# Performance work log

Measured on AMD Instinct MI355X. Metric: run time of the kernel, lower is better.

## Reference

```python
import jax, jax.numpy as jnp
import numpy as np


def _skew(w):
    # w: (..., 3) -> (..., 3, 3)
    wx, wy, wz = w[..., 0], w[..., 1], w[..., 2]
    z = jnp.zeros_like(wx)
    return jnp.stack([
        jnp.stack([z, -wz, wy], axis=-1),
        jnp.stack([wz, z, -wx], axis=-1),
        jnp.stack([-wy, wx, z], axis=-1),
    ], axis=-2)


def exp_se3(xi):
    # xi: (..., 6) se(3) coordinates [w, v] -> (..., 4, 4) SE(3) matrix exponential
    w = xi[..., :3]
    v = xi[..., 3:]
    th2 = jnp.sum(w * w, axis=-1)
    small = th2 < 1e-12
    th2_safe = jnp.where(small, 1.0, th2)
    th = jnp.sqrt(th2_safe)
    # Rodrigues coefficients with small-angle Taylor fallbacks
    A = jnp.where(small, 1.0 - th2 / 6.0, jnp.sin(th) / th)
    B = jnp.where(small, 0.5 - th2 / 24.0, (1.0 - jnp.cos(th)) / th2_safe)
    C = jnp.where(small, 1.0 / 6.0 - th2 / 120.0, (th - jnp.sin(th)) / (th2_safe * th))
    W = _skew(w)
    W2 = W @ W
    I3 = jnp.eye(3, dtype=xi.dtype)
    R = I3 + A[..., None, None] * W + B[..., None, None] * W2
    V = I3 + B[..., None, None] * W + C[..., None, None] * W2
    p = jnp.einsum('...ij,...j->...i', V, v)
    top = jnp.concatenate([R, p[..., None]], axis=-1)            # (..., 3, 4)
    bottom_row = jnp.array([0.0, 0.0, 0.0, 1.0], dtype=xi.dtype)
    bot = jnp.broadcast_to(bottom_row, top.shape[:-2] + (1, 4))  # (..., 1, 4)
    return jnp.concatenate([top, bot], axis=-2)


def setup_inputs() -> dict:
    key = jax.random.key(0)
    k1, k2, k3 = jax.random.split(key, 3)
    nBatch, nJoint = 262144, 24
    x = jax.random.normal(k1, (nBatch, nJoint), dtype=jnp.float32)
    # eta ~ U(-1, 1) per torch init (stdv = 1)
    eta = jax.random.uniform(k2, (nJoint, 6), dtype=jnp.float32, minval=-1.0, maxval=1.0)
    # M_se3 ~ U(-2, 2)
    M_se3 = jax.random.uniform(k3, (1, 6), dtype=jnp.float32, minval=-2.0, maxval=2.0)
    return {"x": x, "eta": eta, "M_se3": M_se3}


def reference(x, eta, M_se3):
    # x: (B, nJoint) joint angles; eta: (nJoint, 6) joint twists (useAdjoint=False);
    # M_se3: (1, 6) home pose in se(3).
    nBatch = x.shape[0]
    joint_twist = eta  # getJointTwist() with useAdjoint=False

    def step(T, inp):
        twist, ang = inp                                  # (6,), (B,)
        E = exp_se3(ang[:, None] * twist[None, :])        # (B, 4, 4)
        return T @ E, None

    T0 = jnp.broadcast_to(jnp.eye(4, dtype=x.dtype), (nBatch, 4, 4))
    T, _ = jax.lax.scan(step, T0, (joint_twist, x.T))
    return T @ exp_se3(M_se3)  # (B,4,4) @ (1,4,4) broadcasts over batch
```

## Files before the change

kernel.cpp:

```cpp
#include <hip/hip_runtime.h>

#define NJ   24
#define BLK  256
#define JREC 5
#define QMF4 (NJ * JREC)
#define NCPY (NJ * JREC + 2)
#define INV4PI 0.07957747154594767f

__global__ __launch_bounds__(BLK, 8)
void poe_main(const float* __restrict__ x,
              const float* __restrict__ eta,
              const float* __restrict__ M,
              float* __restrict__ out,
              int nBatch)
{
    __shared__ float4 sC[NCPY];
    float* sF = (float*)sC;

    const int t = threadIdx.x;
    if (t < NJ) {
        const float w0 = eta[t*6+0], w1 = eta[t*6+1], w2 = eta[t*6+2];
        const float v0 = eta[t*6+3], v1 = eta[t*6+4], v2 = eta[t*6+5];
        const float k  = w0*w0 + w1*w1 + w2*w2;
        const bool  sm = (k < 1e-12f);
        const float invsqk = sm ? 0.0f : rsqrtf(k);
        const float sqk    = k * invsqk;
        const float invk   = invsqk * invsqk;
        const float invk15 = invk * invsqk;
        const float c10 = w1*v2 - w2*v1;
        const float c11 = w2*v0 - w0*v2;
        const float c12 = w0*v1 - w1*v0;
        const float c20 = w1*c12 - w2*c11;
        const float c21 = w2*c10 - w0*c12;
        const float c22 = w0*c11 - w1*c10;
        float* r = sF + t * JREC * 4;
        r[0]  = w0*invsqk;  r[1]  = w1*invsqk;  r[2]  = w2*invsqk;  r[3]  = sqk;
        r[4]  = v0;         r[5]  = v1;         r[6]  = v2;         r[7]  = sqk * INV4PI;
        r[8]  = c10*invk;   r[9]  = c11*invk;   r[10] = c12*invk;   r[11] = 0.0f;
        r[12] = c20*invk15; r[13] = c21*invk15; r[14] = c22*invk15; r[15] = 0.0f;
    } else if (t == NJ) {
        const float w0 = M[0], w1 = M[1], w2 = M[2];
        const float v0 = M[3], v1 = M[4], v2 = M[5];
        const float t2 = w0*w0 + w1*w1 + w2*w2;
        const bool  sm = (t2 < 1e-12f);
        const float t2s  = sm ? 1.0f : t2;
        const float invt = rsqrtf(t2s);
        const float th   = t2s * invt;
        float s, c;
        __sincosf(th, &s, &c);
        const float invt2 = invt * invt;
        const float B = sm ? 0.5f        : (1.0f - c) * invt2;
        const float C = sm ? (1.0f/6.0f) : (th - s) * invt2 * invt;
        float sh, chh;
        __sincosf(0.5f * th, &sh, &chh);
        const float axs = sm ? 0.5f : sh * invt;
        float* r = sF + QMF4 * 4;
        r[0] = sm ? 1.0f : chh;
        r[1] = axs * w0;
        r[2] = axs * w1;
        r[3] = axs * w2;
        const float c10 = w1*v2 - w2*v1, c11 = w2*v0 - w0*v2, c12 = w0*v1 - w1*v0;
        const float c20 = w1*c12 - w2*c11, c21 = w2*c10 - w0*c12, c22 = w0*c11 - w1*c10;
        r[4] = v0 + B*c10 + C*c20;
        r[5] = v1 + B*c11 + C*c21;
        r[6] = v2 + B*c12 + C*c22;
        r[7] = 0.0f;
    }

    const int gid = blockIdx.x * BLK + t;
    const int row = gid >> 2;
    const int q   = gid & 3;
    const bool active = row < nBatch;

    float2 xa = make_float2(0.f,0.f), xb = xa, xc = xa;
    if (active) {
        const float2* xp = (const float2*)(x + (size_t)row * NJ + q * 6);
        xa = xp[0]; xb = xp[1]; xc = xp[2];
    }

    __syncthreads();

    float Qw=1.f, Qx=0.f, Qy=0.f, Qz=0.f;
    float p0=0.f, p1=0.f, p2=0.f;

    const int cbase = q * 6 * JREC;

#define JSTEP(JJ, A_) do {                                                    \
    const float4 A4 = sC[cbase + (JJ)*JREC + 0];                              \
    const float4 B4 = sC[cbase + (JJ)*JREC + 1];                              \
    const float4 C4 = sC[cbase + (JJ)*JREC + 2];                              \
    const float4 D4 = sC[cbase + (JJ)*JREC + 3];                              \
    const float a    = (A_);                                                  \
    const float hrev = a * B4.w;                                              \
    const float sh   = __builtin_amdgcn_sinf(hrev);                           \
    const float ch   = __builtin_amdgcn_cosf(hrev);                           \
    const float s    = 2.0f * sh * ch;                        \
    const float cB   = 2.0f * sh * sh;                        \
    const float phi  = a * A4.w;                                              \
    const float g    = phi - s;                                               \
    const float qj0 = fmaf(a, B4.x, fmaf(cB, C4.x, g * D4.x));                \
    const float qj1 = fmaf(a, B4.y, fmaf(cB, C4.y, g * D4.y));                \
    const float qj2 = fmaf(a, B4.z, fmaf(cB, C4.z, g * D4.z));                \
    const float u10 = Qy*qj2 - Qz*qj1;                                        \
    const float u11 = Qz*qj0 - Qx*qj2;                                        \
    const float u12 = Qx*qj1 - Qy*qj0;                                        \
    const float u20 = Qy*u12 - Qz*u11;                                        \
    const float u21 = Qz*u10 - Qx*u12;                                        \
    const float u22 = Qx*u11 - Qy*u10;                                        \
    const float tw  = 2.0f * Qw;                                              \
    p0 = fmaf(tw, u10, fmaf(2.0f, u20, p0 + qj0));                            \
    p1 = fmaf(tw, u11, fmaf(2.0f, u21, p1 + qj1));                            \
    p2 = fmaf(tw, u12, fmaf(2.0f, u22, p2 + qj2));                            \
    const float ex = sh * A4.x, ey = sh * A4.y, ez = sh * A4.z;               \
    const float nQw = Qw*ch - Qx*ex - Qy*ey - Qz*ez;                          \
    const float nQx = Qw*ex + Qx*ch + Qy*ez - Qz*ey;                          \
    const float nQy = Qw*ey - Qx*ez + Qy*ch + Qz*ex;                          \
    const float nQz = Qw*ez + Qx*ey - Qy*ex + Qz*ch;                          \
    Qw=nQw; Qx=nQx; Qy=nQy; Qz=nQz;                                           \
} while (0)

    JSTEP(0, xa.x); JSTEP(1, xa.y); JSTEP(2, xb.x);
    JSTEP(3, xb.y); JSTEP(4, xc.x); JSTEP(5, xc.y);
#undef JSTEP

#define COMBINE(BIT) do {                                                     \
    const float oQw = __shfl_xor(Qw, BIT), oQx = __shfl_xor(Qx, BIT);         \
    const float oQy = __shfl_xor(Qy, BIT), oQz = __shfl_xor(Qz, BIT);         \
    const float op0 = __shfl_xor(p0, BIT), op1 = __shfl_xor(p1, BIT);         \
    const float op2 = __shfl_xor(p2, BIT);                                    \
    const bool up = (q & (BIT)) != 0;          \
    const float Aw = up ? oQw : Qw, Ax = up ? oQx : Qx;                       \
    const float Ay = up ? oQy : Qy, Az = up ? oQz : Qz;                       \
    const float Ap0 = up ? op0 : p0, Ap1 = up ? op1 : p1, Ap2 = up ? op2 : p2;\
    const float Bw = up ? Qw : oQw, Bx = up ? Qx : oQx;                       \
    const float By = up ? Qy : oQy, Bz = up ? Qz : oQz;                       \
    const float Bp0 = up ? p0 : op0, Bp1 = up ? p1 : op1, Bp2 = up ? p2 : op2;\
    const float u10 = Ay*Bp2 - Az*Bp1;                                        \
    const float u11 = Az*Bp0 - Ax*Bp2;                                        \
    const float u12 = Ax*Bp1 - Ay*Bp0;                                        \
    const float u20 = Ay*u12 - Az*u11;                                        \
    const float u21 = Az*u10 - Ax*u12;                                        \
    const float u22 = Ax*u11 - Ay*u10;                                        \
    const float tw  = 2.0f * Aw;                                              \
    p0 = fmaf(tw, u10, fmaf(2.0f, u20, Ap0 + Bp0));                           \
    p1 = fmaf(tw, u11, fmaf(2.0f, u21, Ap1 + Bp1));                           \
    p2 = fmaf(tw, u12, fmaf(2.0f, u22, Ap2 + Bp2));                           \
    Qw = Aw*Bw - Ax*Bx - Ay*By - Az*Bz;                                       \
    Qx = Aw*Bx + Ax*Bw + Ay*Bz - Az*By;                                       \
    Qy = Aw*By - Ax*Bz + Ay*Bw + Az*Bx;                                       \
    Qz = Aw*Bz + Ax*By - Ay*Bx + Az*Bw;                                       \
} while (0)

    COMBINE(1);
    COMBINE(2);
#undef COMBINE

    {
        const float4 Qm = sC[QMF4];
        const float4 Pm = sC[QMF4 + 1];
        const float u10 = Qy*Pm.z - Qz*Pm.y;
        const float u11 = Qz*Pm.x - Qx*Pm.z;
        const float u12 = Qx*Pm.y - Qy*Pm.x;
        const float u20 = Qy*u12 - Qz*u11;
        const float u21 = Qz*u10 - Qx*u12;
        const float u22 = Qx*u11 - Qy*u10;
        const float tw  = 2.0f * Qw;
        p0 = fmaf(tw, u10, fmaf(2.0f, u20, p0 + Pm.x));
        p1 = fmaf(tw, u11, fmaf(2.0f, u21, p1 + Pm.y));
        p2 = fmaf(tw, u12, fmaf(2.0f, u22, p2 + Pm.z));
        const float nQw = Qw*Qm.x - Qx*Qm.y - Qy*Qm.z - Qz*Qm.w;
        const float nQx = Qw*Qm.y + Qx*Qm.x + Qy*Qm.w - Qz*Qm.z;
        const float nQy = Qw*Qm.z - Qx*Qm.w + Qy*Qm.x + Qz*Qm.y;
        const float nQz = Qw*Qm.w + Qx*Qm.z - Qy*Qm.y + Qz*Qm.x;
        Qw=nQw; Qx=nQx; Qy=nQy; Qz=nQz;
    }

    if (active) {
        const float xx = Qx*Qx, yy = Qy*Qy, zz = Qz*Qz;
        const float xy = Qx*Qy, xz = Qx*Qz, yz = Qy*Qz;
        const float wx = Qw*Qx, wy = Qw*Qy, wz = Qw*Qz;
        const float R00 = 1.0f - 2.0f*(yy + zz);
        const float R01 = 2.0f*(xy - wz);
        const float R02 = 2.0f*(xz + wy);
        const float R10 = 2.0f*(xy + wz);
        const float R11 = 1.0f - 2.0f*(xx + zz);
        const float R12 = 2.0f*(yz - wx);
        const float R20 = 2.0f*(xz - wy);
        const float R21 = 2.0f*(yz + wx);
        const float R22 = 1.0f - 2.0f*(xx + yy);

        float4 mine;
        if      (q == 0) mine = make_float4(R00, R01, R02, p0);
        else if (q == 1) mine = make_float4(R10, R11, R12, p1);
        else if (q == 2) mine = make_float4(R20, R21, R22, p2);
        else             mine = make_float4(0.0f, 0.0f, 0.0f, 1.0f);

        ((float4*)out)[(size_t)row * 4 + q] = mine;
    }
}

extern "C" void kernel_launch(void* const* d_in, const int* in_sizes, int n_in,
                              void* d_out, int out_size, void* d_ws, size_t ws_size,
                              hipStream_t stream)
{
    const float* x   = (const float*)d_in[0];
    const float* eta = (const float*)d_in[1];
    const float* M   = (const float*)d_in[2];
    float* out = (float*)d_out;

    const int nBatch   = in_sizes[0] / NJ;
    const int nThreads = nBatch * 4;
    const int grid     = (nThreads + BLK - 1) / BLK;

    poe_main<<<grid, BLK, 0, stream>>>(x, eta, M, out, nBatch);
}
```

Baseline: 20.36 us.

## Process one batch row per thread instead of four-thread split with shuffle combine

```diff
diff --git a/kernel.cpp b/kernel.cpp
--- a/kernel.cpp
+++ b/kernel.cpp
@@ -2,10 +2,9 @@
 
 #define NJ   24
 #define BLK  256
-#define JREC 5
-#define QMF4 (NJ * JREC)
-#define NCPY (NJ * JREC + 2)
+#define QMF4 (NJ * 4)
 #define INV4PI 0.07957747154594767f
+#define FOURPI 12.566370614359172f
 
 __global__ __launch_bounds__(BLK, 8)
 void poe_main(const float* __restrict__ x,
@@ -14,7 +13,7 @@
               float* __restrict__ out,
               int nBatch)
 {
-    __shared__ float4 sC[NCPY];
+    __shared__ float4 sC[NJ * 4 + 2];
     float* sF = (float*)sC;
 
     const int t = threadIdx.x;
@@ -33,7 +32,7 @@
         const float c20 = w1*c12 - w2*c11;
         const float c21 = w2*c10 - w0*c12;
         const float c22 = w0*c11 - w1*c10;
-        float* r = sF + t * JREC * 4;
+        float* r = sF + t * 16;
         r[0]  = w0*invsqk;  r[1]  = w1*invsqk;  r[2]  = w2*invsqk;  r[3]  = sqk;
         r[4]  = v0;         r[5]  = v1;         r[6]  = v2;         r[7]  = sqk * INV4PI;
         r[8]  = c10*invk;   r[9]  = c11*invk;   r[10] = c12*invk;   r[11] = 0.0f;
@@ -56,9 +55,7 @@
         const float axs = sm ? 0.5f : sh * invt;
         float* r = sF + QMF4 * 4;
         r[0] = sm ? 1.0f : chh;
-        r[1] = axs * w0;
-        r[2] = axs * w1;
-        r[3] = axs * w2;
+        r[1] = axs * w0;  r[2] = axs * w1;  r[3] = axs * w2;
         const float c10 = w1*v2 - w2*v1, c11 = w2*v0 - w0*v2, c12 = w0*v1 - w1*v0;
         const float c20 = w1*c12 - w2*c11, c21 = w2*c10 - w0*c12, c22 = w0*c11 - w1*c10;
         r[4] = v0 + B*c10 + C*c20;
@@ -67,93 +64,83 @@
         r[7] = 0.0f;
     }
 
-    const int gid = blockIdx.x * BLK + t;
-    const int row = gid >> 2;
-    const int q   = gid & 3;
+    const int row = blockIdx.x * BLK + t;
     const bool active = row < nBatch;
 
-    float2 xa = make_float2(0.f,0.f), xb = xa, xc = xa;
+    float4 xz = make_float4(0.f,0.f,0.f,0.f);
+    float4 x0=xz,x1=xz,x2=xz,x3=xz,x4=xz,x5=xz;
     if (active) {
-        const float2* xp = (const float2*)(x + (size_t)row * NJ + q * 6);
-        xa = xp[0]; xb = xp[1]; xc = xp[2];
+        const float4* xr = (const float4*)(x + (size_t)row * NJ);
+        x0=xr[0]; x1=xr[1]; x2=xr[2]; x3=xr[3]; x4=xr[4]; x5=xr[5];
     }
 
     __syncthreads();
 
-    float Qw=1.f, Qx=0.f, Qy=0.f, Qz=0.f;
-    float p0=0.f, p1=0.f, p2=0.f;
+    float Qw, Qx, Qy, Qz, p0, p1, p2;
 
-    const int cbase = q * 6 * JREC;
-
-#define JSTEP(JJ, A_) do {                                                    \
-    const float4 A4 = sC[cbase + (JJ)*JREC + 0];                              \
-    const float4 B4 = sC[cbase + (JJ)*JREC + 1];                              \
-    const float4 C4 = sC[cbase + (JJ)*JREC + 2];                              \
-    const float4 D4 = sC[cbase + (JJ)*JREC + 3];                              \
+#define JSTEP(JJ, A_, FIRST) do {                                             \
+    const float4 A4 = sC[(JJ)*4 + 0];       \
+    const float4 B4 = sC[(JJ)*4 + 1];                                         \
+    const float4 C4 = sC[(JJ)*4 + 2];                                         \
+    const float4 D4 = sC[(JJ)*4 + 3];                                         \
     const float a    = (A_);                                                  \
     const float hrev = a * B4.w;                                              \
     const float sh   = __builtin_amdgcn_sinf(hrev);                           \
     const float ch   = __builtin_amdgcn_cosf(hrev);                           \
     const float s    = 2.0f * sh * ch;                        \
     const float cB   = 2.0f * sh * sh;                        \
-    const float phi  = a * A4.w;                                              \
-    const float g    = phi - s;                                               \
+    const float g    = fmaf(FOURPI, hrev, -s);              \
     const float qj0 = fmaf(a, B4.x, fmaf(cB, C4.x, g * D4.x));                \
     const float qj1 = fmaf(a, B4.y, fmaf(cB, C4.y, g * D4.y));                \
     const float qj2 = fmaf(a, B4.z, fmaf(cB, C4.z, g * D4.z));                \
-    const float u10 = Qy*qj2 - Qz*qj1;                                        \
-    const float u11 = Qz*qj0 - Qx*qj2;                                        \
-    const float u12 = Qx*qj1 - Qy*qj0;                                        \
-    const float u20 = Qy*u12 - Qz*u11;                                        \
-    const float u21 = Qz*u10 - Qx*u12;                                        \
-    const float u22 = Qx*u11 - Qy*u10;                                        \
-    const float tw  = 2.0f * Qw;                                              \
-    p0 = fmaf(tw, u10, fmaf(2.0f, u20, p0 + qj0));                            \
-    p1 = fmaf(tw, u11, fmaf(2.0f, u21, p1 + qj1));                            \
-    p2 = fmaf(tw, u12, fmaf(2.0f, u22, p2 + qj2));                            \
     const float ex = sh * A4.x, ey = sh * A4.y, ez = sh * A4.z;               \
-    const float nQw = Qw*ch - Qx*ex - Qy*ey - Qz*ez;                          \
-    const float nQx = Qw*ex + Qx*ch + Qy*ez - Qz*ey;                          \
-    const float nQy = Qw*ey - Qx*ez + Qy*ch + Qz*ex;                          \
-    const float nQz = Qw*ez + Qx*ey - Qy*ex + Qz*ch;                          \
-    Qw=nQw; Qx=nQx; Qy=nQy; Qz=nQz;                                           \
+    if (FIRST) {                                                              \
+        Qw = ch; Qx = ex; Qy = ey; Qz = ez;                                   \
+        p0 = qj0; p1 = qj1; p2 = qj2;                                         \
+    } else {                                                                  \
+        const float u10 = Qy*qj2 - Qz*qj1;                                    \
+        const float u11 = Qz*qj0 - Qx*qj2;                                    \
+        const float u12 = Qx*qj1 - Qy*qj0;                                    \
+        const float u20 = Qy*u12 - Qz*u11;                                    \
+        const float u21 = Qz*u10 - Qx*u12;                                    \
+        const float u22 = Qx*u11 - Qy*u10;                                    \
+        const float tw  = 2.0f * Qw;                                          \
+        p0 = fmaf(tw, u10, fmaf(2.0f, u20, p0 + qj0));                        \
+        p1 = fmaf(tw, u11, fmaf(2.0f, u21, p1 + qj1));                        \
+        p2 = fmaf(tw, u12, fmaf(2.0f, u22, p2 + qj2));                        \
+        const float nQw = Qw*ch - Qx*ex - Qy*ey - Qz*ez;                      \
+        const float nQx = Qw*ex + Qx*ch + Qy*ez - Qz*ey;                      \
+        const float nQy = Qw*ey - Qx*ez + Qy*ch + Qz*ex;                      \
+        const float nQz = Qw*ez + Qx*ey - Qy*ex + Qz*ch;                      \
+        Qw=nQw; Qx=nQx; Qy=nQy; Qz=nQz;                                       \
+    }                                                                         \
 } while (0)
 
-    JSTEP(0, xa.x); JSTEP(1, xa.y); JSTEP(2, xb.x);
-    JSTEP(3, xb.y); JSTEP(4, xc.x); JSTEP(5, xc.y);
+    JSTEP( 0, x0.x, true);
+    JSTEP( 1, x0.y, false);
+    JSTEP( 2, x0.z, false);
+    JSTEP( 3, x0.w, false);
+    JSTEP( 4, x1.x, false);
+    JSTEP( 5, x1.y, false);
+    JSTEP( 6, x1.z, false);
+    JSTEP( 7, x1.w, false);
+    JSTEP( 8, x2.x, false);
+    JSTEP( 9, x2.y, false);
+    JSTEP(10, x2.z, false);
+    JSTEP(11, x2.w, false);
+    JSTEP(12, x3.x, false);
+    JSTEP(13, x3.y, false);
+    JSTEP(14, x3.z, false);
+    JSTEP(15, x3.w, false);
+    JSTEP(16, x4.x, false);
+    JSTEP(17, x4.y, false);
+    JSTEP(18, x4.z, false);
+    JSTEP(19, x4.w, false);
+    JSTEP(20, x5.x, false);
+    JSTEP(21, x5.y, false);
+    JSTEP(22, x5.z, false);
+    JSTEP(23, x5.w, false);
 #undef JSTEP
-
-#define COMBINE(BIT) do {                                                     \
-    const float oQw = __shfl_xor(Qw, BIT), oQx = __shfl_xor(Qx, BIT);         \
-    const float oQy = __shfl_xor(Qy, BIT), oQz = __shfl_xor(Qz, BIT);         \
-    const float op0 = __shfl_xor(p0, BIT), op1 = __shfl_xor(p1, BIT);         \
-    const float op2 = __shfl_xor(p2, BIT);                                    \
-    const bool up = (q & (BIT)) != 0;          \
-    const float Aw = up ? oQw : Qw, Ax = up ? oQx : Qx;                       \
-    const float Ay = up ? oQy : Qy, Az = up ? oQz : Qz;                       \
-    const float Ap0 = up ? op0 : p0, Ap1 = up ? op1 : p1, Ap2 = up ? op2 : p2;\
-    const float Bw = up ? Qw : oQw, Bx = up ? Qx : oQx;                       \
-    const float By = up ? Qy : oQy, Bz = up ? Qz : oQz;                       \
-    const float Bp0 = up ? p0 : op0, Bp1 = up ? p1 : op1, Bp2 = up ? p2 : op2;\
-    const float u10 = Ay*Bp2 - Az*Bp1;                                        \
-    const float u11 = Az*Bp0 - Ax*Bp2;                                        \
-    const float u12 = Ax*Bp1 - Ay*Bp0;                                        \
-    const float u20 = Ay*u12 - Az*u11;                                        \
-    const float u21 = Az*u10 - Ax*u12;                                        \
-    const float u22 = Ax*u11 - Ay*u10;                                        \
-    const float tw  = 2.0f * Aw;                                              \
-    p0 = fmaf(tw, u10, fmaf(2.0f, u20, Ap0 + Bp0));                           \
-    p1 = fmaf(tw, u11, fmaf(2.0f, u21, Ap1 + Bp1));                           \
-    p2 = fmaf(tw, u12, fmaf(2.0f, u22, Ap2 + Bp2));                           \
-    Qw = Aw*Bw - Ax*Bx - Ay*By - Az*Bz;                                       \
-    Qx = Aw*Bx + Ax*Bw + Ay*Bz - Az*By;                                       \
-    Qy = Aw*By - Ax*Bz + Ay*Bw + Az*Bx;                                       \
-    Qz = Aw*Bz + Ax*By - Ay*Bx + Az*Bw;                                       \
-} while (0)
-
-    COMBINE(1);
-    COMBINE(2);
-#undef COMBINE
 
     {
         const float4 Qm = sC[QMF4];
@@ -179,23 +166,11 @@
         const float xx = Qx*Qx, yy = Qy*Qy, zz = Qz*Qz;
         const float xy = Qx*Qy, xz = Qx*Qz, yz = Qy*Qz;
         const float wx = Qw*Qx, wy = Qw*Qy, wz = Qw*Qz;
-        const float R00 = 1.0f - 2.0f*(yy + zz);
-        const float R01 = 2.0f*(xy - wz);
-        const float R02 = 2.0f*(xz + wy);
-        const float R10 = 2.0f*(xy + wz);
-        const float R11 = 1.0f - 2.0f*(xx + zz);
-        const float R12 = 2.0f*(yz - wx);
-        const float R20 = 2.0f*(xz - wy);
-        const float R21 = 2.0f*(yz + wx);
-        const float R22 = 1.0f - 2.0f*(xx + yy);
-
-        float4 mine;
-        if      (q == 0) mine = make_float4(R00, R01, R02, p0);
-        else if (q == 1) mine = make_float4(R10, R11, R12, p1);
-        else if (q == 2) mine = make_float4(R20, R21, R22, p2);
-        else             mine = make_float4(0.0f, 0.0f, 0.0f, 1.0f);
-
-        ((float4*)out)[(size_t)row * 4 + q] = mine;
+        float4* o = (float4*)(out + (size_t)row * 16);
+        o[0] = make_float4(1.0f-2.0f*(yy+zz), 2.0f*(xy-wz),      2.0f*(xz+wy),      p0);
+        o[1] = make_float4(2.0f*(xy+wz),      1.0f-2.0f*(xx+zz), 2.0f*(yz-wx),      p1);
+        o[2] = make_float4(2.0f*(xz-wy),      2.0f*(yz+wx),      1.0f-2.0f*(xx+yy), p2);
+        o[3] = make_float4(0.0f, 0.0f, 0.0f, 1.0f);
     }
 }
 
@@ -208,9 +183,8 @@
     const float* M   = (const float*)d_in[2];
     float* out = (float*)d_out;
 
-    const int nBatch   = in_sizes[0] / NJ;
-    const int nThreads = nBatch * 4;
-    const int grid     = (nThreads + BLK - 1) / BLK;
+    const int nBatch = in_sizes[0] / NJ;
+    const int grid   = (nBatch + BLK - 1) / BLK;
 
     poe_main<<<grid, BLK, 0, stream>>>(x, eta, M, out, nBatch);
 }
```

Result: slower. 80.19 us (+293.9%).
